# Performance work log

Measured on AMD Instinct MI355X. Metric: run time of the kernel, lower is better.

The kernel has to match this reference:

```python
import jax, jax.numpy as jnp
import numpy as np

D_MODEL = 1024
D_FF = 4096
N_EXPERTS = 4
D_HID = D_MODEL // 2
TOP_K = 2
B, T = 2, 4096


def setup_inputs() -> dict:
    key = jax.random.key(0)
    ks = jax.random.split(key, 10)
    s_in = 1.0 / np.sqrt(D_MODEL)
    s_ff = 1.0 / np.sqrt(D_FF)
    s_h = 1.0 / np.sqrt(D_HID)
    return {
        "x": jax.random.normal(ks[0], (B, T, D_MODEL), jnp.float32),
        # stacked expert FFN params [E, ...]
        "w1": jax.random.normal(ks[1], (N_EXPERTS, D_MODEL, D_FF), jnp.float32) * s_in,
        "b1": jnp.zeros((N_EXPERTS, D_FF), jnp.float32),
        "w2": jax.random.normal(ks[2], (N_EXPERTS, D_FF, D_MODEL), jnp.float32) * s_ff,
        "b2": jnp.zeros((N_EXPERTS, D_MODEL), jnp.float32),
        # router MLP params
        "wr1": jax.random.normal(ks[3], (D_MODEL, D_HID), jnp.float32) * s_in,
        "br1": jnp.zeros((D_HID,), jnp.float32),
        "wr2": jax.random.normal(ks[4], (D_HID, N_EXPERTS), jnp.float32) * s_h,
        "br2": jnp.zeros((N_EXPERTS,), jnp.float32),
    }


def _gelu(x):
    return jax.nn.gelu(x, approximate=False)  # torch nn.GELU default is exact erf


def reference(x, w1, b1, w2, b2, wr1, br1, wr2, br2):
    # Router: 2-layer MLP -> logits [B,T,E]
    h = _gelu(jnp.einsum('btd,dh->bth', x, wr1) + br1)
    logits = jnp.einsum('bth,he->bte', h, wr2) + br2
    # top-k masked softmax over experts
    top_vals, _ = jax.lax.top_k(logits, TOP_K)
    thresh = top_vals[..., -1:]
    masked = jnp.where(logits >= thresh, logits, -jnp.inf)
    gate = jax.nn.softmax(masked, axis=-1)  # [B,T,E], zeros off top-k
    # dense all-experts FFN: hid [B,T,E,d_ff]
    hid = _gelu(jnp.einsum('btd,edf->btef', x, w1) + b1)
    expert_outs = jnp.einsum('btef,efd->bted', hid, w2) + b2  # [B,T,E,d_model]
    out = jnp.einsum('bte,bted->btd', gate, expert_outs)
    return out, gate
```

## Files before the change

### kernel.cpp

```cpp
#include <hip/hip_runtime.h>

#define NTOK 8192
#define DM 1024
#define DF 4096
#define DH 512
#define NE 4
#define SLOTS (NTOK * 2)
#define NYT_MAX 132

typedef unsigned short ushort_t;
typedef short bf16x8 __attribute__((ext_vector_type(8)));
typedef float f32x4 __attribute__((ext_vector_type(4)));

__device__ __forceinline__ unsigned short f2bf(float f) {
    unsigned int u = __float_as_uint(f);
    u += 0x7FFFu + ((u >> 16) & 1u);
    return (unsigned short)(u >> 16);
}
__device__ __forceinline__ float bf2f(unsigned short h) {
    return __uint_as_float(((unsigned int)h) << 16);
}
__device__ __forceinline__ float gelu_exact(float x) {
    return 0.5f * x * (1.0f + erff(x * 0.7071067811865476f));
}
__device__ __forceinline__ float gelu_fast(float x) {
    float u = 1.5957691216057308f * (x + 0.044715f * x * x * x);
    return x / (1.0f + __expf(-u));
}
__device__ __forceinline__ void gload16(const void* g, void* l) {
    __builtin_amdgcn_global_load_lds((__attribute__((address_space(1))) void*)(g),
                                     (__attribute__((address_space(3))) void*)(l), 16, 0, 0);
}
__device__ __forceinline__ int swz(int b) { return b ^ (((b >> 7) & 3) << 4); }
__device__ __forceinline__ int imin(int a, int b) { return a < b ? a : b; }

__global__ __launch_bounds__(256) void k_cast_split(const float* __restrict__ in,
                                                    ushort_t* __restrict__ hi,
                                                    ushort_t* __restrict__ lo, int n4) {
    int i = blockIdx.x * 256 + threadIdx.x;
    if (i >= n4) return;
    float4 v = ((const float4*)in)[i];
    ushort4 h, l;
    h.x = f2bf(v.x); l.x = f2bf(v.x - bf2f(h.x));
    h.y = f2bf(v.y); l.y = f2bf(v.y - bf2f(h.y));
    h.z = f2bf(v.z); l.z = f2bf(v.z - bf2f(h.z));
    h.w = f2bf(v.w); l.w = f2bf(v.w - bf2f(h.w));
    ((ushort4*)hi)[i] = h;
    ((ushort4*)lo)[i] = l;
}

template <bool SPLIT>
__global__ __launch_bounds__(256) void k_tcast(const float* __restrict__ in,
                                               ushort_t* __restrict__ oh,
                                               ushort_t* __restrict__ ol, int K, int N) {
    __shared__ float t[64][65];
    size_t base = (size_t)blockIdx.z * K * N;
    const float* src = in + base;
    int k0 = blockIdx.y * 64, n0 = blockIdx.x * 64;
    int tx = threadIdx.x & 63, ty = threadIdx.x >> 6;
#pragma unroll
    for (int i = 0; i < 16; i++) {
        int r = ty + i * 4;
        t[r][tx] = src[(size_t)(k0 + r) * N + n0 + tx];
    }
    __syncthreads();
#pragma unroll
    for (int i = 0; i < 16; i++) {
        int nn = ty + i * 4;
        float v = t[tx][nn];
        unsigned short hv = f2bf(v);
        size_t o = base + (size_t)(n0 + nn) * K + k0 + tx;
        oh[o] = hv;
        if (SPLIT) ol[o] = f2bf(v - bf2f(hv));
    }
}

__global__ __launch_bounds__(256) void k_rgemm(
    const ushort_t* __restrict__ A0, const ushort_t* __restrict__ B0,
    const ushort_t* __restrict__ A1, const ushort_t* __restrict__ B1,
    const ushort_t* __restrict__ A2, const ushort_t* __restrict__ B2,
    int K, int N, const float* __restrict__ bias, float* __restrict__ outF)
{
    __shared__ ushort_t lA[4096];
    __shared__ ushort_t lB[4096];
    int row0 = blockIdx.y * 128, col0 = blockIdx.x * 128;
    int tid = threadIdx.x, lane = tid & 63, wv = tid >> 6;
    int wr = wv >> 1, wc = wv & 1;
    int r15 = lane & 15, hq = lane >> 4;

    f32x4 z = {0.f, 0.f, 0.f, 0.f};
    f32x4 acc[4][4];
#pragma unroll
    for (int m = 0; m < 4; m++)
#pragma unroll
        for (int n = 0; n < 4; n++) acc[m][n] = z;

    int d0 = tid * 16, d1 = d0 + 4096;
    int u0 = swz(d0), u1 = swz(d1);
    int rA0 = u0 >> 6, ko0 = ((u0 >> 4) & 3) * 8;
    int rA1 = u1 >> 6, ko1 = ((u1 >> 4) & 3) * 8;
    char* ldA0 = (char*)lA + wv * 1024;
    char* ldA1 = (char*)lA + 4096 + wv * 1024;
    char* ldB0 = (char*)lB + wv * 1024;
    char* ldB1 = (char*)lB + 4096 + wv * 1024;

#pragma unroll
    for (int p = 0; p < 3; p++) {
        const ushort_t* A = (p == 0) ? A0 : ((p == 1) ? A1 : A2);
        const ushort_t* B = (p == 0) ? B0 : ((p == 1) ? B1 : B2);
        const ushort_t* Ab0 = A + (size_t)(row0 + rA0) * K + ko0;
        const ushort_t* Ab1 = A + (size_t)(row0 + rA1) * K + ko1;
        const ushort_t* Bb0 = B + (size_t)(col0 + rA0) * K + ko0;
        const ushort_t* Bb1 = B + (size_t)(col0 + rA1) * K + ko1;
        for (int kt = 0; kt < K; kt += 32) {
            gload16(Ab0 + kt, ldA0);
            gload16(Ab1 + kt, ldA1);
            gload16(Bb0 + kt, ldB0);
            gload16(Bb1 + kt, ldB1);
            __syncthreads();
            bf16x8 af[4], bfr[4];
#pragma unroll
            for (int m = 0; m < 4; m++) {
                int u = ((wr * 64 + m * 16 + r15) << 6) + (hq << 4);
                af[m] = *(const bf16x8*)((const char*)lA + swz(u));
            }
#pragma unroll
            for (int n = 0; n < 4; n++) {
                int u = ((wc * 64 + n * 16 + r15) << 6) + (hq << 4);
                bfr[n] = *(const bf16x8*)((const char*)lB + swz(u));
            }
#pragma unroll
            for (int m = 0; m < 4; m++)
#pragma unroll
                for (int n = 0; n < 4; n++)
                    acc[m][n] = __builtin_amdgcn_mfma_f32_16x16x32_bf16(af[m], bfr[n], acc[m][n], 0, 0, 0);
            __syncthreads();
        }
    }
#pragma unroll
    for (int m = 0; m < 4; m++)
#pragma unroll
        for (int q = 0; q < 4; q++) {
            int row = row0 + wr * 64 + m * 16 + hq * 4 + q;
#pragma unroll
            for (int n = 0; n < 4; n++) {
                int col = col0 + wc * 64 + n * 16 + r15;
                outF[(size_t)row * N + col] = gelu_exact(acc[m][n][q] + bias[col]);
            }
        }
}

template <int MODE>
__global__ __launch_bounds__(512, 4) void k_egemm(
    const ushort_t* __restrict__ A0, const ushort_t* __restrict__ B0,
    const float* __restrict__ bias, const float* __restrict__ gate,
    const int* __restrict__ idx, const int4* __restrict__ tiles,
    const int* __restrict__ meta,
    ushort_t* __restrict__ ghid, float* __restrict__ outA)
{
    constexpr int K = (MODE == 1) ? DM : DF;
    constexpr int NFULL = (MODE == 1) ? DF : DM;
    constexpr int NXT = NFULL / 256;
    constexpr int nwg = NXT * NYT_MAX;
    constexpr int q8 = nwg / 8;

    int bid = blockIdx.x;
    int wgid = (bid & 7) * q8 + (bid >> 3);
    int xt = wgid / NYT_MAX, yt = wgid % NYT_MAX;
    if (yt >= meta[0]) return;
    int4 ti = tiles[yt];
    int e = ti.x, rstart = ti.y, rows = ti.z, gbase = ti.w;
    int col0 = xt * 256;

    __shared__ ushort_t lA[2][4096];
    __shared__ ushort_t lB[2][8192];
    int tid = threadIdx.x, lane = tid & 63, wv = tid >> 6;
    int wr = wv >> 2, wc = wv & 3;
    int r15 = lane & 15, hq = lane >> 4;

    f32x4 z = {0.f, 0.f, 0.f, 0.f};
    f32x4 acc[4][4];
#pragma unroll
    for (int m = 0; m < 4; m++)
#pragma unroll
        for (int n = 0; n < 4; n++) acc[m][n] = z;

    int u = swz(tid * 16);
    int rA = u >> 6;
    int ko = ((u >> 4) & 3) * 8;
    const ushort_t *Ab, *Bb0, *Bb1;
    if (MODE == 1) {
        int tok = idx[e * NTOK + rstart + imin(rA, rows - 1)];
        Ab = A0 + (size_t)tok * K + ko;
    } else {
        Ab = A0 + (size_t)(gbase + imin(rA, rows - 1)) * K + ko;
    }
    Bb0 = B0 + ((size_t)e * NFULL + col0 + rA) * K + ko;
    Bb1 = B0 + ((size_t)e * NFULL + col0 + 128 + rA) * K + ko;

    char* dstA = (char*)&lA[0][0];
    char* dstB = (char*)&lB[0][0];

    auto stage = [&](int b, int kt) {
        gload16(Ab + kt, dstA + b * 8192 + wv * 1024);
        gload16(Bb0 + kt, dstB + b * 16384 + wv * 1024);
        gload16(Bb1 + kt, dstB + b * 16384 + 8192 + wv * 1024);
    };
    auto compute = [&](int b) {
        const char* pa = (const char*)&lA[b][0];
        const char* pb = (const char*)&lB[b][0];
        bf16x8 af[4], bfr[4];
#pragma unroll
        for (int m = 0; m < 4; m++) {
            int ub = ((wr * 64 + m * 16 + r15) << 6) + (hq << 4);
            af[m] = *(const bf16x8*)(pa + swz(ub));
        }
#pragma unroll
        for (int n = 0; n < 4; n++) {
            int ub = ((wc * 64 + n * 16 + r15) << 6) + (hq << 4);
            bfr[n] = *(const bf16x8*)(pb + swz(ub));
        }
#pragma unroll
        for (int m = 0; m < 4; m++)
#pragma unroll
            for (int n = 0; n < 4; n++)
                acc[m][n] = __builtin_amdgcn_mfma_f32_16x16x32_bf16(af[m], bfr[n], acc[m][n], 0, 0, 0);
    };

    stage(0, 0);
    __syncthreads();
    int cur = 0;
    for (int kt = 32; kt < K; kt += 32) {
        stage(cur ^ 1, kt);
        compute(cur);
        __syncthreads();
        cur ^= 1;
    }
    compute(cur);

    if (MODE == 1) {
#pragma unroll
        for (int m = 0; m < 4; m++)
#pragma unroll
            for (int q = 0; q < 4; q++) {
                int lr = wr * 64 + m * 16 + hq * 4 + q;
                if (lr < rows) {
                    int token = idx[e * NTOK + rstart + lr];
                    float g = gate[token * 4 + e];
                    size_t rb = (size_t)(gbase + lr) * NFULL;
#pragma unroll
                    for (int n = 0; n < 4; n++) {
                        int col = col0 + wc * 64 + n * 16 + r15;
                        float v = gelu_fast(acc[m][n][q] + bias[(size_t)e * NFULL + col]) * g;
                        ghid[rb + col] = f2bf(v);
                    }
                }
            }
    } else {
#pragma unroll
        for (int m = 0; m < 4; m++)
#pragma unroll
            for (int q = 0; q < 4; q++) {
                int lr = wr * 64 + m * 16 + hq * 4 + q;
                if (lr < rows) {
                    int token = idx[e * NTOK + rstart + lr];
#pragma unroll
                    for (int n = 0; n < 4; n++) {
                        int col = col0 + wc * 64 + n * 16 + r15;
                        atomicAdd(&outA[(size_t)token * NFULL + col], acc[m][n][q]);
                    }
                }
            }
    }
}

__global__ __launch_bounds__(256) void k_gate(const float* __restrict__ h,
                                              const float* __restrict__ wr2,
                                              const float* __restrict__ br2,
                                              float* __restrict__ gate,
                                              int* __restrict__ cnt,
                                              int* __restrict__ idx) {
    int t = blockIdx.x * 4 + (threadIdx.x >> 6);
    int lane = threadIdx.x & 63;
    const float* hr = h + (size_t)t * DH;
    const float4* w4 = (const float4*)wr2;
    float gx = 0.f, gy = 0.f, gz = 0.f, gw = 0.f;
#pragma unroll
    for (int j = 0; j < 8; j++) {
        int k = lane * 8 + j;
        float hv = hr[k];
        float4 w = w4[k];
        gx += hv * w.x; gy += hv * w.y; gz += hv * w.z; gw += hv * w.w;
    }
#pragma unroll
    for (int off = 32; off > 0; off >>= 1) {
        gx += __shfl_xor(gx, off);
        gy += __shfl_xor(gy, off);
        gz += __shfl_xor(gz, off);
        gw += __shfl_xor(gw, off);
    }
    if (lane == 0) {
        float ls[4];
        ls[0] = gx + br2[0]; ls[1] = gy + br2[1]; ls[2] = gz + br2[2]; ls[3] = gw + br2[3];
        int i1 = 0; float m1 = ls[0];
#pragma unroll
        for (int i = 1; i < 4; i++) if (ls[i] > m1) { m1 = ls[i]; i1 = i; }
        int i2 = -1; float m2 = -1e30f;
#pragma unroll
        for (int i = 0; i < 4; i++) if (i != i1 && ls[i] > m2) { m2 = ls[i]; i2 = i; }
        float e0 = (ls[0] >= m2) ? expf(ls[0] - m1) : 0.f;
        float e1 = (ls[1] >= m2) ? expf(ls[1] - m1) : 0.f;
        float e2 = (ls[2] >= m2) ? expf(ls[2] - m1) : 0.f;
        float e3 = (ls[3] >= m2) ? expf(ls[3] - m1) : 0.f;
        float iz = 1.f / (e0 + e1 + e2 + e3);
        float4 g = {e0 * iz, e1 * iz, e2 * iz, e3 * iz};
        ((float4*)gate)[t] = g;
        int s0 = atomicAdd(&cnt[i1], 1);
        idx[i1 * NTOK + s0] = t;
        int s1 = atomicAdd(&cnt[i2], 1);
        idx[i2 * NTOK + s1] = t;
    }
}

__global__ void k_tiles(const int* __restrict__ cnt, int4* __restrict__ tiles,
                        int* __restrict__ meta) {
    if (threadIdx.x != 0 || blockIdx.x != 0) return;
    int base = 0, nt = 0;
    for (int e = 0; e < NE; e++) {
        int c = cnt[e];
        for (int r = 0; r < c; r += 128) {
            int4 ti;
            ti.x = e; ti.y = r; ti.z = (c - r < 128) ? (c - r) : 128; ti.w = base + r;
            tiles[nt++] = ti;
        }
        base += c;
    }
    meta[0] = nt;
}

__global__ __launch_bounds__(256) void k_init_out(const float* __restrict__ gate,
                                                  const float* __restrict__ b2,
                                                  float* __restrict__ out) {
    int i = blockIdx.x * 256 + threadIdx.x;
    int t = i >> 8;
    int c4 = i & 255;
    float4 g = ((const float4*)gate)[t];
    const float4* b = (const float4*)b2;
    float4 v0 = b[c4], v1 = b[256 + c4], v2 = b[512 + c4], v3 = b[768 + c4];
    float4 o;
    o.x = g.x * v0.x + g.y * v1.x + g.z * v2.x + g.w * v3.x;
    o.y = g.x * v0.y + g.y * v1.y + g.z * v2.y + g.w * v3.y;
    o.z = g.x * v0.z + g.y * v1.z + g.z * v2.z + g.w * v3.z;
    o.w = g.x * v0.w + g.y * v1.w + g.z * v2.w + g.w * v3.w;
    ((float4*)out)[i] = o;
}

extern "C" void kernel_launch(void* const* d_in, const int* in_sizes, int n_in,
                              void* d_out, int out_size, void* d_ws, size_t ws_size,
                              hipStream_t stream) {
    const float* x   = (const float*)d_in[0];
    const float* w1  = (const float*)d_in[1];
    const float* b1  = (const float*)d_in[2];
    const float* w2  = (const float*)d_in[3];
    const float* b2  = (const float*)d_in[4];
    const float* wr1 = (const float*)d_in[5];
    const float* br1 = (const float*)d_in[6];
    const float* wr2 = (const float*)d_in[7];
    const float* br2 = (const float*)d_in[8];
    float* out  = (float*)d_out;
    float* gate = out + (size_t)NTOK * DM;

    char* p = (char*)d_ws;
    auto take = [&](size_t bytes) { char* r = p; p += (bytes + 255) & ~(size_t)255; return r; };
    ushort_t* xh    = (ushort_t*)take((size_t)NTOK * DM * 2);
    ushort_t* w1T   = (ushort_t*)take((size_t)NE * DF * DM * 2);
    ushort_t* w2T   = (ushort_t*)take((size_t)NE * DM * DF * 2);
    ushort_t* wr1Th = (ushort_t*)take((size_t)DH * DM * 2);
    ushort_t* wr1Tl = (ushort_t*)take((size_t)DH * DM * 2);
    int*      cnt   = (int*)take(64);
    int*      idx   = (int*)take((size_t)NE * NTOK * 4);
    int4*     tiles = (int4*)take(144 * 16);
    int*      meta  = (int*)take(64);
    char*     region = take((size_t)SLOTS * DF * 2);
    ushort_t* xl    = (ushort_t*)region;
    float*    h     = (float*)(region + (size_t)NTOK * DM * 2);
    ushort_t* ghid  = (ushort_t*)region;

    hipMemsetAsync(cnt, 0, 64, stream);

    k_cast_split<<<NTOK * DM / 4 / 256, 256, 0, stream>>>(x, xh, xl, NTOK * DM / 4);
    k_tcast<false><<<dim3(DF / 64, DM / 64, NE), 256, 0, stream>>>(w1, w1T, nullptr, DM, DF);
    k_tcast<false><<<dim3(DM / 64, DF / 64, NE), 256, 0, stream>>>(w2, w2T, nullptr, DF, DM);
    k_tcast<true ><<<dim3(DH / 64, DM / 64, 1),  256, 0, stream>>>(wr1, wr1Th, wr1Tl, DM, DH);

    k_rgemm<<<dim3(DH / 128, NTOK / 128), 256, 0, stream>>>(
        xh, wr1Th, xh, wr1Tl, xl, wr1Th, DM, DH, br1, h);
    k_gate<<<NTOK / 4, 256, 0, stream>>>(h, wr2, br2, gate, cnt, idx);
    k_tiles<<<1, 64, 0, stream>>>(cnt, tiles, meta);
    k_init_out<<<NTOK * DM / 4 / 256, 256, 0, stream>>>(gate, b2, out);

    k_egemm<1><<<(DF / 256) * NYT_MAX, 512, 0, stream>>>(
        xh, w1T, b1, gate, idx, tiles, meta, ghid, nullptr);
    k_egemm<2><<<(DM / 256) * NYT_MAX, 512, 0, stream>>>(
        ghid, w2T, nullptr, gate, idx, tiles, meta, nullptr, out);
}
```

Measured before the change: 949.0 us.

## Triple-buffer LDS with fine-grained vmcnt waits in router and expert GEMMs

```diff
diff --git a/kernel.cpp b/kernel.cpp
--- a/kernel.cpp
+++ b/kernel.cpp
@@ -33,6 +33,11 @@
 }
 __device__ __forceinline__ int swz(int b) { return b ^ (((b >> 7) & 3) << 4); }
 __device__ __forceinline__ int imin(int a, int b) { return a < b ? a : b; }
+
+#define WAIT_VM(N) asm volatile("s_waitcnt vmcnt(" #N ")" ::: "memory")
+#define WAIT_LGKM0() asm volatile("s_waitcnt lgkmcnt(0)" ::: "memory")
+#define SBAR() __builtin_amdgcn_s_barrier()
+#define SCHED0() __builtin_amdgcn_sched_barrier(0)
 
 __global__ __launch_bounds__(256) void k_cast_split(const float* __restrict__ in,
                                                     ushort_t* __restrict__ hi,
@@ -81,8 +86,8 @@
     const ushort_t* __restrict__ A2, const ushort_t* __restrict__ B2,
     int K, int N, const float* __restrict__ bias, float* __restrict__ outF)
 {
-    __shared__ ushort_t lA[4096];
-    __shared__ ushort_t lB[4096];
+    __shared__ ushort_t lA[3][4096];
+    __shared__ ushort_t lB[3][4096];
     int row0 = blockIdx.y * 128, col0 = blockIdx.x * 128;
     int tid = threadIdx.x, lane = tid & 63, wv = tid >> 6;
     int wr = wv >> 1, wc = wv & 1;
@@ -99,12 +104,9 @@
     int u0 = swz(d0), u1 = swz(d1);
     int rA0 = u0 >> 6, ko0 = ((u0 >> 4) & 3) * 8;
     int rA1 = u1 >> 6, ko1 = ((u1 >> 4) & 3) * 8;
-    char* ldA0 = (char*)lA + wv * 1024;
-    char* ldA1 = (char*)lA + 4096 + wv * 1024;
-    char* ldB0 = (char*)lB + wv * 1024;
-    char* ldB1 = (char*)lB + 4096 + wv * 1024;
-
-#pragma unroll
+    int nstep = K / 32;
+
+#pragma unroll 1
     for (int p = 0; p < 3; p++) {
         const ushort_t* A = (p == 0) ? A0 : ((p == 1) ? A1 : A2);
         const ushort_t* B = (p == 0) ? B0 : ((p == 1) ? B1 : B2);
@@ -112,31 +114,54 @@
         const ushort_t* Ab1 = A + (size_t)(row0 + rA1) * K + ko1;
         const ushort_t* Bb0 = B + (size_t)(col0 + rA0) * K + ko0;
         const ushort_t* Bb1 = B + (size_t)(col0 + rA1) * K + ko1;
-        for (int kt = 0; kt < K; kt += 32) {
-            gload16(Ab0 + kt, ldA0);
-            gload16(Ab1 + kt, ldA1);
-            gload16(Bb0 + kt, ldB0);
-            gload16(Bb1 + kt, ldB1);
-            __syncthreads();
+
+        auto stage = [&](int b, int s) {
+            int kt = s * 32;
+            char* la = (char*)lA + b * 8192;
+            char* lb = (char*)lB + b * 8192;
+            gload16(Ab0 + kt, la + wv * 1024);
+            gload16(Ab1 + kt, la + 4096 + wv * 1024);
+            gload16(Bb0 + kt, lb + wv * 1024);
+            gload16(Bb1 + kt, lb + 4096 + wv * 1024);
+        };
+        auto compute = [&](int b) {
+            const char* pa = (const char*)lA + b * 8192;
+            const char* pb = (const char*)lB + b * 8192;
             bf16x8 af[4], bfr[4];
 #pragma unroll
-            for (int m = 0; m < 4; m++) {
-                int u = ((wr * 64 + m * 16 + r15) << 6) + (hq << 4);
-                af[m] = *(const bf16x8*)((const char*)lA + swz(u));
-            }
-#pragma unroll
-            for (int n = 0; n < 4; n++) {
-                int u = ((wc * 64 + n * 16 + r15) << 6) + (hq << 4);
-                bfr[n] = *(const bf16x8*)((const char*)lB + swz(u));
-            }
+            for (int m = 0; m < 4; m++)
+                af[m] = *(const bf16x8*)(pa + swz(((wr * 64 + m * 16 + r15) << 6) + (hq << 4)));
+#pragma unroll
+            for (int n = 0; n < 4; n++)
+                bfr[n] = *(const bf16x8*)(pb + swz(((wc * 64 + n * 16 + r15) << 6) + (hq << 4)));
+            __builtin_amdgcn_s_setprio(1);
 #pragma unroll
             for (int m = 0; m < 4; m++)
 #pragma unroll
                 for (int n = 0; n < 4; n++)
                     acc[m][n] = __builtin_amdgcn_mfma_f32_16x16x32_bf16(af[m], bfr[n], acc[m][n], 0, 0, 0);
-            __syncthreads();
+            __builtin_amdgcn_s_setprio(0);
+        };
+
+        stage(0, 0); stage(1, 1); stage(2, 2);
+        int cur = 0;
+#pragma unroll 1
+        for (int s = 0; s < nstep - 3; s++) {
+            WAIT_VM(8); SBAR(); SCHED0();
+            compute(cur);
+            WAIT_LGKM0(); SCHED0(); SBAR(); SCHED0();
+            stage(cur, s + 3);
+            cur = (cur == 2) ? 0 : cur + 1;
         }
-    }
+        WAIT_VM(8); SBAR(); SCHED0();
+        compute(cur); cur = (cur == 2) ? 0 : cur + 1;
+        WAIT_VM(4); SBAR(); SCHED0();
+        compute(cur); cur = (cur == 2) ? 0 : cur + 1;
+        WAIT_VM(0); SBAR(); SCHED0();
+        compute(cur);
+        WAIT_LGKM0(); SCHED0(); SBAR(); SCHED0();
+    }
+
 #pragma unroll
     for (int m = 0; m < 4; m++)
 #pragma unroll
@@ -163,6 +188,7 @@
     constexpr int NXT = NFULL / 256;
     constexpr int nwg = NXT * NYT_MAX;
     constexpr int q8 = nwg / 8;
+    constexpr int NSTEP = K / 32;
 
     int bid = blockIdx.x;
     int wgid = (bid & 7) * q8 + (bid >> 3);
@@ -172,8 +198,8 @@
     int e = ti.x, rstart = ti.y, rows = ti.z, gbase = ti.w;
     int col0 = xt * 256;
 
-    __shared__ ushort_t lA[2][4096];
-    __shared__ ushort_t lB[2][8192];
+    __shared__ ushort_t lA[3][4096];
+    __shared__ ushort_t lB[3][8192];
     int tid = threadIdx.x, lane = tid & 63, wv = tid >> 6;
     int wr = wv >> 2, wc = wv & 3;
     int r15 = lane & 15, hq = lane >> 4;
@@ -198,44 +224,46 @@
     Bb0 = B0 + ((size_t)e * NFULL + col0 + rA) * K + ko;
     Bb1 = B0 + ((size_t)e * NFULL + col0 + 128 + rA) * K + ko;
 
-    char* dstA = (char*)&lA[0][0];
-    char* dstB = (char*)&lB[0][0];
-
-    auto stage = [&](int b, int kt) {
-        gload16(Ab + kt, dstA + b * 8192 + wv * 1024);
-        gload16(Bb0 + kt, dstB + b * 16384 + wv * 1024);
-        gload16(Bb1 + kt, dstB + b * 16384 + 8192 + wv * 1024);
+    auto stage = [&](int b, int s) {
+        int kt = s * 32;
+        gload16(Ab + kt, (char*)lA + b * 8192 + wv * 1024);
+        gload16(Bb0 + kt, (char*)lB + b * 16384 + wv * 1024);
+        gload16(Bb1 + kt, (char*)lB + b * 16384 + 8192 + wv * 1024);
     };
     auto compute = [&](int b) {
-        const char* pa = (const char*)&lA[b][0];
-        const char* pb = (const char*)&lB[b][0];
+        const char* pa = (const char*)lA + b * 8192;
+        const char* pb = (const char*)lB + b * 16384;
         bf16x8 af[4], bfr[4];
 #pragma unroll
-        for (int m = 0; m < 4; m++) {
-            int ub = ((wr * 64 + m * 16 + r15) << 6) + (hq << 4);
-            af[m] = *(const bf16x8*)(pa + swz(ub));
-        }
-#pragma unroll
-        for (int n = 0; n < 4; n++) {
-            int ub = ((wc * 64 + n * 16 + r15) << 6) + (hq << 4);
-            bfr[n] = *(const bf16x8*)(pb + swz(ub));
-        }
+        for (int m = 0; m < 4; m++)
+            af[m] = *(const bf16x8*)(pa + swz(((wr * 64 + m * 16 + r15) << 6) + (hq << 4)));
+#pragma unroll
+        for (int n = 0; n < 4; n++)
+            bfr[n] = *(const bf16x8*)(pb + swz(((wc * 64 + n * 16 + r15) << 6) + (hq << 4)));
+        __builtin_amdgcn_s_setprio(1);
 #pragma unroll
         for (int m = 0; m < 4; m++)
 #pragma unroll
             for (int n = 0; n < 4; n++)
                 acc[m][n] = __builtin_amdgcn_mfma_f32_16x16x32_bf16(af[m], bfr[n], acc[m][n], 0, 0, 0);
+        __builtin_amdgcn_s_setprio(0);
     };
 
-    stage(0, 0);
-    __syncthreads();
+    stage(0, 0); stage(1, 1); stage(2, 2);
     int cur = 0;
-    for (int kt = 32; kt < K; kt += 32) {
-        stage(cur ^ 1, kt);
+#pragma unroll 1
+    for (int s = 0; s < NSTEP - 3; s++) {
+        WAIT_VM(6); SBAR(); SCHED0();
         compute(cur);
-        __syncthreads();
-        cur ^= 1;
-    }
+        WAIT_LGKM0(); SCHED0(); SBAR(); SCHED0();
+        stage(cur, s + 3);
+        cur = (cur == 2) ? 0 : cur + 1;
+    }
+    WAIT_VM(6); SBAR(); SCHED0();
+    compute(cur); cur = (cur == 2) ? 0 : cur + 1;
+    WAIT_VM(3); SBAR(); SCHED0();
+    compute(cur); cur = (cur == 2) ? 0 : cur + 1;
+    WAIT_VM(0); SBAR(); SCHED0();
     compute(cur);
 
     if (MODE == 1) {
```

Result: no change. 941.9 us (-0.7%).
